# Optimization experiments

Hardware: AMD Instinct MI355X
Metric: run time of the kernel (lower is better)

The kernel has to match this reference:

```python
import jax, jax.numpy as jnp
import numpy as np

IN_CH = [32, 48, 96, 136, 232]
SIZES = [128, 64, 32, 16, 8]
C = 256      # FPN channels (compound_coef=0)
A = 9        # anchors per location
NC = 10      # num_classes
B = 8
BN_EPS = 1e-5


def conv2d(x, w, b, pad):
    # x: [B,Cin,H,W], w: [Cout,Cin,kh,kw]
    y = jax.lax.conv_general_dilated(
        x, w, window_strides=(1, 1), padding=[(pad, pad), (pad, pad)],
        dimension_numbers=("NCHW", "OIHW", "NCHW"))
    return y + b[None, :, None, None]


def bn_eval(x, g, bt, m, v):
    inv = g / jnp.sqrt(v + BN_EPS)
    return x * inv[None, :, None, None] + (bt - m * inv)[None, :, None, None]


def upsample_nearest(x, th, tw):
    fh = th // x.shape[2]
    fw = tw // x.shape[3]
    return jnp.repeat(jnp.repeat(x, fh, axis=2), fw, axis=3)


def run_head(feats, w1, b1, g, bt, m, v, w2, b2, out_dim):
    outs = []
    for f in feats:
        h = jax.nn.relu(bn_eval(conv2d(f, w1, b1, 1), g, bt, m, v))
        h = conv2d(h, w2, b2, 0)                       # [B, A*out_dim, H, W]
        Bb, _, H, W = h.shape
        h = h.transpose(0, 2, 3, 1).reshape(Bb, H * W * A, out_dim)
        outs.append(h)
    return jnp.concatenate(outs, axis=1)               # [B, total_anchors, out_dim]


def _forward(f1, f2, f3, f4, f5,
             lat_w1, lat_w2, lat_w3, lat_w4, lat_w5, lat_b,
             fpn_w, fpn_b,
             cls_w1, cls_b1, cls_g, cls_bt, cls_m, cls_v, cls_w2, cls_b2,
             reg_w1, reg_b1, reg_g, reg_bt, reg_m, reg_v, reg_w2, reg_b2):
    feats = [f1, f2, f3, f4, f5]
    lat_ws = [lat_w1, lat_w2, lat_w3, lat_w4, lat_w5]
    # lateral 1x1 convs
    laterals = [conv2d(feats[i], lat_ws[i], lat_b[i], 0) for i in range(5)]
    # top-down pathway with nearest upsampling
    for i in range(4, 0, -1):
        th, tw = laterals[i - 1].shape[2], laterals[i - 1].shape[3]
        laterals[i - 1] = laterals[i - 1] + upsample_nearest(laterals[i], th, tw)
    # 3x3 fpn convs
    fpn_feats = [conv2d(laterals[i], fpn_w[i], fpn_b[i], 1) for i in range(5)]
    cls = run_head(fpn_feats, cls_w1, cls_b1, cls_g, cls_bt, cls_m, cls_v, cls_w2, cls_b2, NC)
    reg = run_head(fpn_feats, reg_w1, reg_b1, reg_g, reg_bt, reg_m, reg_v, reg_w2, reg_b2, 4)
    return jnp.concatenate([reg, cls], axis=2)          # [B, total_anchors, 4+NC]


def setup_inputs() -> dict:
    key = jax.random.key(0)
    ks = jax.random.split(key, 16)
    d = {}
    for i, (ch, s) in enumerate(zip(IN_CH, SIZES)):
        d[f"f{i+1}"] = jax.random.normal(ks[i], (B, ch, s, s), jnp.float32)
    for i, ch in enumerate(IN_CH):
        std = float(np.sqrt(2.0 / C))
        d[f"lat_w{i+1}"] = jax.random.normal(ks[5 + i], (C, ch, 1, 1), jnp.float32) * std
    d["lat_b"] = jnp.zeros((5, C), jnp.float32)
    d["fpn_w"] = jax.random.normal(ks[10], (5, C, C, 3, 3), jnp.float32) * float(np.sqrt(2.0 / (9 * C)))
    d["fpn_b"] = jnp.zeros((5, C), jnp.float32)
    d["cls_w1"] = jax.random.normal(ks[11], (C, C, 3, 3), jnp.float32) * float(np.sqrt(2.0 / (9 * C)))
    d["cls_b1"] = jnp.zeros((C,), jnp.float32)
    d["cls_g"] = jnp.ones((C,), jnp.float32)
    d["cls_bt"] = jnp.zeros((C,), jnp.float32)
    d["cls_m"] = jnp.zeros((C,), jnp.float32)
    d["cls_v"] = jnp.ones((C,), jnp.float32)
    d["cls_w2"] = jax.random.normal(ks[12], (A * NC, C, 1, 1), jnp.float32) * float(np.sqrt(2.0 / (A * NC)))
    d["cls_b2"] = jnp.zeros((A * NC,), jnp.float32)
    d["reg_w1"] = jax.random.normal(ks[13], (C, C, 3, 3), jnp.float32) * float(np.sqrt(2.0 / (9 * C)))
    d["reg_b1"] = jnp.zeros((C,), jnp.float32)
    d["reg_g"] = jnp.ones((C,), jnp.float32)
    d["reg_bt"] = jnp.zeros((C,), jnp.float32)
    d["reg_m"] = jnp.zeros((C,), jnp.float32)
    d["reg_v"] = jnp.ones((C,), jnp.float32)
    d["reg_w2"] = jax.random.normal(ks[14], (A * 4, C, 1, 1), jnp.float32) * float(np.sqrt(2.0 / (A * 4)))
    d["reg_b2"] = jnp.zeros((A * 4,), jnp.float32)
    return d


def reference(f1, f2, f3, f4, f5,
              lat_w1, lat_w2, lat_w3, lat_w4, lat_w5, lat_b,
              fpn_w, fpn_b,
              cls_w1, cls_b1, cls_g, cls_bt, cls_m, cls_v, cls_w2, cls_b2,
              reg_w1, reg_b1, reg_g, reg_bt, reg_m, reg_v, reg_w2, reg_b2):
    return _forward(f1, f2, f3, f4, f5,
                    lat_w1, lat_w2, lat_w3, lat_w4, lat_w5, lat_b,
                    fpn_w, fpn_b,
                    cls_w1, cls_b1, cls_g, cls_bt, cls_m, cls_v, cls_w2, cls_b2,
                    reg_w1, reg_b1, reg_g, reg_bt, reg_m, reg_v, reg_w2, reg_b2)
```

## Files before the change

kernel.cpp:

```cpp
#include <hip/hip_runtime.h>


typedef unsigned short ush;
typedef __attribute__((ext_vector_type(8))) short v8s;
typedef __attribute__((ext_vector_type(4))) float v4f;

constexpr int TOTAL_ANCH = 196416;

#define VMW(n) asm volatile("s_waitcnt vmcnt(" #n ")" ::: "memory")
#define LGW()  asm volatile("s_waitcnt lgkmcnt(0)" ::: "memory")

__device__ __forceinline__ ush f2bf(float x) {
    unsigned u = __builtin_bit_cast(unsigned, x);
    u += 0x7FFFu + ((u >> 16) & 1u);
    return (ush)(u >> 16);
}
__device__ __forceinline__ float bf2f(ush h) {
    unsigned u = ((unsigned)h) << 16;
    return __builtin_bit_cast(float, u);
}
__device__ __forceinline__ void splitf(float x, ush& hi, ush& lo) {
    hi = f2bf(x);
    lo = f2bf(x - bf2f(hi));
}

__device__ __forceinline__ void gl_lds16(const ush* g, short* l) {
    __builtin_amdgcn_global_load_lds(
        (const __attribute__((address_space(1))) unsigned*)(const void*)g,
        (__attribute__((address_space(3))) unsigned*)l, 16, 0, 0);
}

struct Lvl3 {
    const ush* xh; const ush* xl;
    ush* yh; ush* yl;
    const float* bias;
    int wofs, logS, logHW, bstart;
};
struct Tab3 { Lvl3 l[4]; };

struct LvlS {
    const ush* xh; const ush* xl;
    int abase, logHW, bstart, ibase;
};
struct TabS { LvlS l[4]; };

template <int OM, bool BNR>
__global__ __launch_bounds__(512, 2)
void conv3f(Tab3 T,
            const ush* __restrict__ Wh, const ush* __restrict__ Wl,
            const float* __restrict__ bng, const float* __restrict__ bnb,
            const float* __restrict__ bnm, const float* __restrict__ bnv)
{
    constexpr int K = 2304, KC = 72;

    const int nwg = gridDim.x;
    const int flat = blockIdx.x;
    const int xcd = flat & 7, sidx = flat >> 3;
    const int q = nwg >> 3, r8 = nwg & 7;
    const int nf = (xcd < r8 ? xcd * (q + 1) : r8 * (q + 1) + (xcd - r8) * q) + sidx;

    int li = 0;
    if (nf >= T.l[1].bstart) li = 1;
    if (nf >= T.l[2].bstart) li = 2;
    if (nf >= T.l[3].bstart) li = 3;
    const int logS = T.l[li].logS, logHW = T.l[li].logHW;
    const int S = 1 << logS, HW = 1 << logHW, P = S + 2;
    const ush* __restrict__ Xh = T.l[li].xh;
    const ush* __restrict__ Xl = T.l[li].xl;
    ush* __restrict__ Yh = T.l[li].yh;
    ush* __restrict__ Yl = T.l[li].yl;
    const float* __restrict__ bias = T.l[li].bias;
    const int wofs = T.l[li].wofs;
    const int n0 = (nf - T.l[li].bstart) * 128;

    __shared__ __align__(16) short lds[3][24576];

    const int tid = threadIdx.x;
    const int lane = tid & 63, w = tid >> 6;
    const int wm = w & 3, wn = w >> 2;
    const int l15 = lane & 15, l4 = lane >> 4;
    const int lr = lane >> 2, ls = lane & 3;
    const int sw = ls ^ ((lr >> 1) & 3);

    const int role = w >> 1, part = w & 1;
    const ush* gsrc = role == 0 ? Wh + wofs : role == 1 ? Wl + wofs
                    : role == 2 ? Xh : Xl;
    const int poff = role < 2 ? role * 8192 : 16384 + (role - 2) * 4096;

    int sb[8];
    if (role < 2) {
#pragma unroll
        for (int t = 0; t < 8; ++t)
            sb[t] = (part * 128 + t * 16 + lr) * K + sw * 8;
    } else {
#pragma unroll
        for (int t = 0; t < 4; ++t) {
            const int p = n0 + part * 64 + t * 16 + lr;
            const int bb = p >> logHW, hw = p & (HW - 1);
            const int oh = hw >> logS, ow = hw & (S - 1);
            sb[t] = ((bb * P + oh + 1) * P + ow + 1) * 256 + sw * 8;
        }
    }

    auto stage = [&](int u, int c, int h) {
        short* db = &lds[0][0] + u * 24576 + poff;
        if (role < 2) {
            const int coff = c * 32;
#pragma unroll
            for (int k = 0; k < 4; ++k) {
                const int t = h * 4 + k;
                gl_lds16(gsrc + (sb[t] + coff), db + part * 4096 + t * 512);
            }
        } else {
            const int rs = c >> 3;
            const int rr = (rs * 11) >> 5;
            const int ss = rs - 3 * rr;
            const int coff = ((rr - 1) * P + (ss - 1)) * 256 + (c & 7) * 32;
#pragma unroll
            for (int k = 0; k < 2; ++k) {
                const int t = h * 2 + k;
                gl_lds16(gsrc + (sb[t] + coff), db + part * 2048 + t * 512);
            }
        }
    };

    const int slr = (l4 ^ ((l15 >> 1) & 3)) * 8;
    int aoff[4], boff[4];
#pragma unroll
    for (int i = 0; i < 4; ++i) aoff[i] = (wm * 64 + i * 16 + l15) * 32 + slr;
#pragma unroll
    for (int j = 0; j < 4; ++j) boff[j] = (wn * 64 + j * 16 + l15) * 32 + slr;

    v4f acc[4][4] = {};

    stage(0, 0, 0); stage(0, 0, 1);
    stage(1, 1, 0); stage(1, 1, 1);
    if (role < 2) { VMW(8); } else { VMW(4); }
    __builtin_amdgcn_sched_barrier(0);
    __builtin_amdgcn_s_barrier();

    int cur = 0, nst = 2;
    for (int c = 0; c < KC; ++c) {
        const bool pf = (c + 2) < KC;
        const short* bb = &lds[0][0] + cur * 24576;

        v8s ah[4], al[4], bh[4], bl[4];
#pragma unroll
        for (int i = 0; i < 4; ++i) {
            ah[i] = *(const v8s*)(bb + aoff[i]);
            al[i] = *(const v8s*)(bb + 8192 + aoff[i]);
        }
#pragma unroll
        for (int j = 0; j < 2; ++j) {
            bh[j] = *(const v8s*)(bb + 16384 + boff[j]);
            bl[j] = *(const v8s*)(bb + 20480 + boff[j]);
        }
        if (pf) stage(nst, c + 2, 0);
        __builtin_amdgcn_s_barrier();
        LGW();
        __builtin_amdgcn_sched_barrier(0);
        __builtin_amdgcn_s_setprio(1);
#pragma unroll
        for (int j = 0; j < 2; ++j)
#pragma unroll
            for (int i = 0; i < 4; ++i) {
                acc[i][j] = __builtin_amdgcn_mfma_f32_16x16x32_bf16(ah[i], bh[j], acc[i][j], 0, 0, 0);
                acc[i][j] = __builtin_amdgcn_mfma_f32_16x16x32_bf16(ah[i], bl[j], acc[i][j], 0, 0, 0);
                acc[i][j] = __builtin_amdgcn_mfma_f32_16x16x32_bf16(al[i], bh[j], acc[i][j], 0, 0, 0);
            }
        __builtin_amdgcn_s_setprio(0);
        __builtin_amdgcn_s_barrier();

#pragma unroll
        for (int j = 2; j < 4; ++j) {
            bh[j] = *(const v8s*)(bb + 16384 + boff[j]);
            bl[j] = *(const v8s*)(bb + 20480 + boff[j]);
        }
        if (pf) stage(nst, c + 2, 1);
        __builtin_amdgcn_s_barrier();
        LGW();
        __builtin_amdgcn_sched_barrier(0);
        __builtin_amdgcn_s_setprio(1);
#pragma unroll
        for (int j = 2; j < 4; ++j)
#pragma unroll
            for (int i = 0; i < 4; ++i) {
                acc[i][j] = __builtin_amdgcn_mfma_f32_16x16x32_bf16(ah[i], bh[j], acc[i][j], 0, 0, 0);
                acc[i][j] = __builtin_amdgcn_mfma_f32_16x16x32_bf16(ah[i], bl[j], acc[i][j], 0, 0, 0);
                acc[i][j] = __builtin_amdgcn_mfma_f32_16x16x32_bf16(al[i], bh[j], acc[i][j], 0, 0, 0);
            }
        __builtin_amdgcn_s_setprio(0);
        if (pf) { if (role < 2) { VMW(8); } else { VMW(4); } }
        else    { VMW(0); }
        __builtin_amdgcn_sched_barrier(0);
        __builtin_amdgcn_s_barrier();

        cur = cur == 2 ? 0 : cur + 1;
        nst = nst == 2 ? 0 : nst + 1;
    }

#pragma unroll
    for (int i = 0; i < 4; ++i) {
        const int co = wm * 64 + i * 16 + l4 * 4;
        float sc[4], sh[4];
#pragma unroll
        for (int e = 0; e < 4; ++e) {
            if (BNR) {
                const float inv = bng[co + e] * rsqrtf(bnv[co + e] + 1e-5f);
                sc[e] = inv;
                sh[e] = (bias[co + e] - bnm[co + e]) * inv + bnb[co + e];
            } else { sc[e] = 1.f; sh[e] = bias[co + e]; }
        }
#pragma unroll
        for (int j = 0; j < 4; ++j) {
            const int ncol = n0 + wn * 64 + j * 16 + l15;
            const int b  = ncol >> logHW;
            const int hw = ncol & (HW - 1);
            float val[4];
#pragma unroll
            for (int e = 0; e < 4; ++e) {
                float x = acc[i][j][e] * sc[e] + sh[e];
                if (BNR) x = fmaxf(x, 0.f);
                val[e] = x;
            }
            int pidx;
            if (OM == 0) {
                const int oh = hw >> logS, ow = hw & (S - 1);
                pidx = (b * P + oh + 1) * P + ow + 1;
            } else {
                pidx = ncol;
            }
            const int addr = pidx * 256 + co;
            ush hs[4], ls2[4];
#pragma unroll
            for (int e = 0; e < 4; ++e) splitf(val[e], hs[e], ls2[e]);
            *(uint2*)&Yh[addr] = make_uint2(hs[0] | ((unsigned)hs[1] << 16),
                                            hs[2] | ((unsigned)hs[3] << 16));
            *(uint2*)&Yl[addr] = make_uint2(ls2[0] | ((unsigned)ls2[1] << 16),
                                            ls2[2] | ((unsigned)ls2[3] << 16));
        }
    }
}

template <int DD>
__global__ __launch_bounds__(256, 3)
void conv_sf(TabS T, const ush* __restrict__ Wh, const ush* __restrict__ Wl,
             const float* __restrict__ bias, float* __restrict__ out)
{
    constexpr int K = 256, KC = 8, Cout = 9 * DD;
    constexpr int coloff = (DD == 10) ? 4 : 0;

    const int nwg = gridDim.x;
    const int flat = blockIdx.x;
    const int xcd = flat & 7, sidx = flat >> 3;
    const int q = nwg >> 3, r8 = nwg & 7;
    const int nf = (xcd < r8 ? xcd * (q + 1) : r8 * (q + 1) + (xcd - r8) * q) + sidx;

    int li = 0;
    if (nf >= T.l[1].bstart) li = 1;
    if (nf >= T.l[2].bstart) li = 2;
    if (nf >= T.l[3].bstart) li = 3;
    const int logHW = T.l[li].logHW;
    const int HW = 1 << logHW;
    const ush* __restrict__ Xh = T.l[li].xh;
    const ush* __restrict__ Xl = T.l[li].xl;
    const int abase = T.l[li].abase, ibase = T.l[li].ibase;
    const int n0 = (nf - T.l[li].bstart) * 128;

    __shared__ short lds[4][128][32];

    const int tid = threadIdx.x;
    const int lane = tid & 63;
    const int w = tid >> 6;
    const int wm = w & 1, wn = w >> 1;
    const int l15 = lane & 15, l4 = lane >> 4;
    const int lr = lane >> 2, ls = lane & 3;
    const int sw = ls ^ ((lr >> 1) & 3);
    const ush* gsrc = (w == 0) ? Wh : (w == 1) ? Wl : (w == 2) ? Xh : Xl;
    int sb[8];
    if (w < 2) {
#pragma unroll
        for (int t = 0; t < 8; ++t)
            sb[t] = (t * 16 + lr) * K + sw * 8;
    } else {
#pragma unroll
        for (int t = 0; t < 8; ++t)
            sb[t] = (n0 + t * 16 + lr) * 256 + sw * 8;
    }
    short* mypl = &lds[w][0][0];
    const int slA = (l4 ^ ((l15 >> 1) & 3)) * 8;

    v4f acc[4][4] = {};

    for (int c = 0; c < KC; ++c) {
        const int coff = c * 32;
#pragma unroll
        for (int t = 0; t < 8; ++t)
            gl_lds16(gsrc + (sb[t] + coff), mypl + t * 512);

        __syncthreads();

        v8s ah[4], al[4];
#pragma unroll
        for (int i = 0; i < 4; ++i) {
            ah[i] = *(const v8s*)&lds[0][wm * 64 + i * 16 + l15][slA];
            al[i] = *(const v8s*)&lds[1][wm * 64 + i * 16 + l15][slA];
        }
#pragma unroll
        for (int j = 0; j < 4; ++j) {
            const v8s bh = *(const v8s*)&lds[2][wn * 64 + j * 16 + l15][slA];
            const v8s bl = *(const v8s*)&lds[3][wn * 64 + j * 16 + l15][slA];
#pragma unroll
            for (int i = 0; i < 4; ++i) {
                acc[i][j] = __builtin_amdgcn_mfma_f32_16x16x32_bf16(ah[i], bh, acc[i][j], 0, 0, 0);
                acc[i][j] = __builtin_amdgcn_mfma_f32_16x16x32_bf16(ah[i], bl, acc[i][j], 0, 0, 0);
                acc[i][j] = __builtin_amdgcn_mfma_f32_16x16x32_bf16(al[i], bh, acc[i][j], 0, 0, 0);
            }
        }
        __syncthreads();
    }

#pragma unroll
    for (int i = 0; i < 4; ++i) {
        const int co = wm * 64 + i * 16 + l4 * 4;
        float sh[4];
#pragma unroll
        for (int e = 0; e < 4; ++e)
            sh[e] = (co + e < Cout) ? bias[co + e] : 0.f;
#pragma unroll
        for (int j = 0; j < 4; ++j) {
            const int ncol = n0 + wn * 64 + j * 16 + l15;
            const int b  = ncol >> logHW;
            const int hw = ncol & (HW - 1);
#pragma unroll
            for (int e = 0; e < 4; ++e) {
                const int c2 = co + e;
                if (c2 < Cout) {
                    const float val = acc[i][j][e] + sh[e];
                    const int a = c2 / DD, cl = c2 - a * DD;
                    out[(size_t)((b + ibase) * TOTAL_ANCH + abase + hw * 9 + a) * 14
                        + coloff + cl] = val;
                }
            }
        }
    }
}

template <int KS, int OM, bool BNR, int DD>
__global__ __launch_bounds__(256, 3)
void conv_mfma(const ush* __restrict__ Xh, const ush* __restrict__ Xl,
               const ush* __restrict__ Wh, const ush* __restrict__ Wl,
               const float* __restrict__ bias,
               ush* __restrict__ Yh, ush* __restrict__ Yl,
               int K, int logS, int logHW, int Kin)
{
    const int tid = threadIdx.x;

    const int nwg  = gridDim.x * gridDim.y;
    const int flat = blockIdx.y * gridDim.x + blockIdx.x;
    const int xcd = flat & 7, sidx = flat >> 3;
    const int q = nwg >> 3, r8 = nwg & 7;
    const int nf = (xcd < r8 ? xcd * (q + 1) : r8 * (q + 1) + (xcd - r8) * q) + sidx;
    int bx, by;
    if (gridDim.y == 2) { bx = nf >> 1; by = nf & 1; }
    else                { bx = nf;      by = 0;      }

    const int n0  = bx * 128;
    const int co0 = by * 128;
    const int S = 1 << logS, HW = 1 << logHW, P = S + 2;

    __shared__ short lds[4][128][32];

    const int lane = tid & 63;
    const int w = tid >> 6;
    const int wm = w & 1, wn = w >> 1;
    const int l15 = lane & 15, l4 = lane >> 4;

    const int lr = lane >> 2, ls = lane & 3;
    const int sw = ls ^ ((lr >> 1) & 3);
    const ush* gsrc = (w == 0) ? Wh : (w == 1) ? Wl : (w == 2) ? Xh : Xl;
    int sb[8];
    if (w < 2) {
#pragma unroll
        for (int t = 0; t < 8; ++t)
            sb[t] = (co0 + t * 16 + lr) * K + sw * 8;
    } else {
#pragma unroll
        for (int t = 0; t < 8; ++t) {
            const int p = n0 + t * 16 + lr;
            sb[t] = p * Kin + sw * 8;
        }
    }
    short* mypl = &lds[w][0][0];

    const int KC = K >> 5;
    const int slA = (l4 ^ ((l15 >> 1) & 3)) * 8;

    v4f acc[4][4] = {};

    for (int c = 0; c < KC; ++c) {
        const int coff = c * 32;
#pragma unroll
        for (int t = 0; t < 8; ++t)
            gl_lds16(gsrc + (sb[t] + coff), mypl + t * 512);

        __syncthreads();

        v8s ah[4], al[4];
#pragma unroll
        for (int i = 0; i < 4; ++i) {
            ah[i] = *(const v8s*)&lds[0][wm * 64 + i * 16 + l15][slA];
            al[i] = *(const v8s*)&lds[1][wm * 64 + i * 16 + l15][slA];
        }
#pragma unroll
        for (int j = 0; j < 4; ++j) {
            const v8s bh = *(const v8s*)&lds[2][wn * 64 + j * 16 + l15][slA];
            const v8s bl = *(const v8s*)&lds[3][wn * 64 + j * 16 + l15][slA];
#pragma unroll
            for (int i = 0; i < 4; ++i) {
                acc[i][j] = __builtin_amdgcn_mfma_f32_16x16x32_bf16(ah[i], bh, acc[i][j], 0, 0, 0);
                acc[i][j] = __builtin_amdgcn_mfma_f32_16x16x32_bf16(ah[i], bl, acc[i][j], 0, 0, 0);
                acc[i][j] = __builtin_amdgcn_mfma_f32_16x16x32_bf16(al[i], bh, acc[i][j], 0, 0, 0);
            }
        }
        __syncthreads();
    }

#pragma unroll
    for (int i = 0; i < 4; ++i) {
        const int cob = wm * 64 + i * 16 + l4 * 4;
        const int co  = co0 + cob;
        float sh[4];
#pragma unroll
        for (int e = 0; e < 4; ++e) sh[e] = bias[co + e];
#pragma unroll
        for (int j = 0; j < 4; ++j) {
            const int ncol = n0 + wn * 64 + j * 16 + l15;
            const int b  = ncol >> logHW;
            const int hw = ncol & (HW - 1);
            float val[4];
#pragma unroll
            for (int e = 0; e < 4; ++e) val[e] = acc[i][j][e] + sh[e];
            int pidx;
            if (OM == 0) {
                const int oh = hw >> logS, ow = hw & (S - 1);
                pidx = (b * P + oh + 1) * P + ow + 1;
            } else {
                pidx = ncol;
            }
            const int addr = pidx * 256 + co;
            ush hs[4], ls2[4];
#pragma unroll
            for (int e = 0; e < 4; ++e) splitf(val[e], hs[e], ls2[e]);
            *(uint2*)&Yh[addr] = make_uint2(hs[0] | ((unsigned)hs[1] << 16),
                                            hs[2] | ((unsigned)hs[3] << 16));
            *(uint2*)&Yl[addr] = make_uint2(ls2[0] | ((unsigned)ls2[1] << 16),
                                            ls2[2] | ((unsigned)ls2[3] << 16));
        }
    }
}


__global__ void w3_prep(const float* __restrict__ W, ush* __restrict__ wh,
                        ush* __restrict__ wl, int total) {
    const int idx = blockIdx.x * 256 + threadIdx.x;
    if (idx >= total) return;
    const int co5 = idx / 2304;
    const int kk  = idx - co5 * 2304;
    const int rs = kk >> 8, ci = kk & 255;
    splitf(W[(co5 * 256 + ci) * 9 + rs], wh[idx], wl[idx]);
}

__global__ void w1_prep(const float* __restrict__ W, ush* __restrict__ wh,
                        ush* __restrict__ wl, int Cin, int Kp, int Cout, int total) {
    const int idx = blockIdx.x * 256 + threadIdx.x;
    if (idx >= total) return;
    const int co = idx / Kp;
    const int k  = idx - co * Kp;
    const float x = (co < Cout && k < Cin) ? W[co * Cin + k] : 0.f;
    splitf(x, wh[idx], wl[idx]);
}

__global__ void in_prep(const float* __restrict__ f, ush* __restrict__ xh,
                        ush* __restrict__ xl, int Cin, int Kp, int logHW, int total) {
    const int idx = blockIdx.x * 256 + threadIdx.x;
    if (idx >= total) return;
    const int c = idx % Kp;
    const int n = idx / Kp;
    const int b  = n >> logHW;
    const int hw = n & ((1 << logHW) - 1);
    const float x = (c < Cin) ? f[((b * Cin + c) << logHW) + hw] : 0.f;
    splitf(x, xh[idx], xl[idx]);
}

__global__ void upsample_hl(ush* __restrict__ fh, ush* __restrict__ fl,
                            const ush* __restrict__ ch, const ush* __restrict__ cl2,
                            int logSf, int total) {
    const int idx = blockIdx.x * 256 + threadIdx.x;
    if (idx >= total) return;
    const int ci = idx & 255;
    const int r  = idx >> 8;
    const int Sf = 1 << logSf;
    const int wf = r & (Sf - 1);
    const int hf = (r >> logSf) & (Sf - 1);
    const int b  = r >> (2 * logSf);
    const int Pf = Sf + 2, Pc = (Sf >> 1) + 2;
    const int fi = ((b * Pf + hf + 1) * Pf + wf + 1) * 256 + ci;
    const int cx = ((b * Pc + (hf >> 1) + 1) * Pc + (wf >> 1) + 1) * 256 + ci;
    const float x = bf2f(fh[fi]) + bf2f(fl[fi]) + bf2f(ch[cx]) + bf2f(cl2[cx]);
    splitf(x, fh[fi], fl[fi]);
}

__global__ void ring_zero(ush* __restrict__ yh, ush* __restrict__ yl, int S, int total) {
    const int idx = blockIdx.x * 256 + threadIdx.x;
    if (idx >= total) return;
    const int ci = idx & 255;
    const int r  = idx >> 8;
    const int P = S + 2;
    const int ring = 4 * P - 4;
    const int pr = r % ring;
    const int b  = r / ring;
    int ph, pw;
    if (pr < P)            { ph = 0;     pw = pr; }
    else if (pr < 2 * P)   { ph = P - 1; pw = pr - P; }
    else { const int q = pr - 2 * P; ph = 1 + (q >> 1); pw = (q & 1) ? (P - 1) : 0; }
    const int a = ((b * P + ph) * P + pw) * 256 + ci;
    yh[a] = 0; yl[a] = 0;
}


extern "C" void kernel_launch(void* const* d_in, const int* in_sizes, int n_in,
                              void* d_out, int out_size, void* d_ws, size_t ws_size,
                              hipStream_t stream)
{
    const float* f[5];     const float* lat_w[5];
    for (int i = 0; i < 5; ++i) f[i] = (const float*)d_in[i];
    for (int i = 0; i < 5; ++i) lat_w[i] = (const float*)d_in[5 + i];
    const float* lat_b  = (const float*)d_in[10];
    const float* fpn_w  = (const float*)d_in[11];
    const float* fpn_b  = (const float*)d_in[12];
    const float* cls_w1 = (const float*)d_in[13];
    const float* cls_b1 = (const float*)d_in[14];
    const float* cls_g  = (const float*)d_in[15];
    const float* cls_bt = (const float*)d_in[16];
    const float* cls_m  = (const float*)d_in[17];
    const float* cls_v  = (const float*)d_in[18];
    const float* cls_w2 = (const float*)d_in[19];
    const float* cls_b2 = (const float*)d_in[20];
    const float* reg_w1 = (const float*)d_in[21];
    const float* reg_b1 = (const float*)d_in[22];
    const float* reg_g  = (const float*)d_in[23];
    const float* reg_bt = (const float*)d_in[24];
    const float* reg_m  = (const float*)d_in[25];
    const float* reg_v  = (const float*)d_in[26];
    const float* reg_w2 = (const float*)d_in[27];
    const float* reg_b2 = (const float*)d_in[28];

    float* out = (float*)d_out;
    ush*   ws16 = (ush*)d_ws;

    static const int S_[5]     = {128, 64, 32, 16, 8};
    static const int logS_[5]  = {7, 6, 5, 4, 3};
    static const int logHW_[5] = {14, 12, 10, 8, 6};
    static const int HW_[5]    = {16384, 4096, 1024, 256, 64};
    static const int Cin_[5]   = {32, 48, 96, 136, 232};
    static const int Kp_[5]    = {32, 64, 96, 160, 256};
    static const int abase_[5] = {0, 147456, 184320, 193536, 195840};
    constexpr int BIG = 0x7fffffff;

    size_t off = 0;
    auto alloc = [&](size_t elems) {
        ush* p = ws16 + off;
        off += (elems + 63) & ~(size_t)63;
        return p;
    };

    ush *lat_h[5], *lat_l[5];
    for (int i = 0; i < 5; ++i) {
        const int P = S_[i] + 2;
        const size_t e = (size_t)2048 * P * P;
        lat_h[i] = alloc(e); lat_l[i] = alloc(e);
    }
    const size_t lat_bytes = off * sizeof(ush);

    const size_t ARENA_E = (size_t)2 * 4 * 130 * 130 * 256;
    ush* arena = alloc(ARENA_E);

    ush* fw_h = alloc((size_t)5 * 256 * 2304); ush* fw_l = alloc((size_t)5 * 256 * 2304);
    ush* cw_h = alloc(256 * 2304);             ush* cw_l = alloc(256 * 2304);
    ush* rw_h = alloc(256 * 2304);             ush* rw_l = alloc(256 * 2304);
    ush *lw_h[5], *lw_l[5];
    for (int i = 0; i < 5; ++i) { lw_h[i] = alloc(256 * Kp_[i]); lw_l[i] = alloc(256 * Kp_[i]); }
    ush* c2_h = alloc(128 * 256); ush* c2_l = alloc(128 * 256);
    ush* r2_h = alloc(128 * 256); ush* r2_l = alloc(128 * 256);

    hipMemsetAsync(ws16, 0, lat_bytes, stream);

    {
        int t = 5 * 256 * 2304;
        w3_prep<<<dim3((t + 255) / 256), 256, 0, stream>>>(fpn_w, fw_h, fw_l, t);
        t = 256 * 2304;
        w3_prep<<<dim3((t + 255) / 256), 256, 0, stream>>>(cls_w1, cw_h, cw_l, t);
        w3_prep<<<dim3((t + 255) / 256), 256, 0, stream>>>(reg_w1, rw_h, rw_l, t);
        for (int i = 0; i < 5; ++i) {
            t = 256 * Kp_[i];
            w1_prep<<<dim3((t + 255) / 256), 256, 0, stream>>>(lat_w[i], lw_h[i], lw_l[i], Cin_[i], Kp_[i], 256, t);
        }
        t = 128 * 256;
        w1_prep<<<dim3((t + 255) / 256), 256, 0, stream>>>(cls_w2, c2_h, c2_l, 256, 256, 90, t);
        w1_prep<<<dim3((t + 255) / 256), 256, 0, stream>>>(reg_w2, r2_h, r2_l, 256, 256, 36, t);
    }

    for (int i = 0; i < 5; ++i) {
        const int N = 8 * HW_[i];
        const int t = N * Kp_[i];
        ush* xh = arena;
        ush* xl = arena + (size_t)N * Kp_[i];
        in_prep<<<dim3((t + 255) / 256), 256, 0, stream>>>(f[i], xh, xl, Cin_[i], Kp_[i], logHW_[i], t);
        conv_mfma<1, 0, false, 0><<<dim3(N / 128, 2), 256, 0, stream>>>(
            xh, xl, lw_h[i], lw_l[i], lat_b + i * 256,
            lat_h[i], lat_l[i],
            Kp_[i], logS_[i], logHW_[i], Kp_[i]);
    }

    for (int i = 4; i >= 1; --i) {
        const int t = 8 * HW_[i - 1] * 256;
        upsample_hl<<<dim3((t + 255) / 256), 256, 0, stream>>>(
            lat_h[i - 1], lat_l[i - 1], lat_h[i], lat_l[i], logS_[i - 1], t);
    }

    ush *fpn_h4[5], *fpn_l4[5];
    {
        size_t o = 0;
        for (int i = 1; i < 5; ++i) {
            const int P = S_[i] + 2;
            fpn_h4[i] = arena + o; o += (size_t)2048 * P * P;
            fpn_l4[i] = arena + o; o += (size_t)2048 * P * P;
        }
    }
    for (int i = 1; i < 5; ++i) {
        const int P = S_[i] + 2;
        const int rt = 8 * (4 * P - 4) * 256;
        ring_zero<<<dim3((rt + 255) / 256), 256, 0, stream>>>(fpn_h4[i], fpn_l4[i], S_[i], rt);
    }
    static const int bstart4[4] = {0, 256, 320, 336};

    {
        Tab3 T{};
        for (int k = 0; k < 4; ++k) {
            const int i = k + 1;
            T.l[k] = Lvl3{ lat_h[i], lat_l[i], fpn_h4[i], fpn_l4[i],
                           fpn_b + i * 256, i * 256 * 2304,
                           logS_[i], logHW_[i], bstart4[k] };
        }
        conv3f<0, false><<<dim3(340), 512, 0, stream>>>(
            T, fw_h, fw_l, nullptr, nullptr, nullptr, nullptr);
    }
    {
        Tab3 T{};
        for (int k = 0; k < 4; ++k) {
            const int i = k + 1;
            T.l[k] = Lvl3{ fpn_h4[i], fpn_l4[i], lat_h[i], lat_l[i],
                           cls_b1, 0, logS_[i], logHW_[i], bstart4[k] };
        }
        conv3f<1, true><<<dim3(340), 512, 0, stream>>>(
            T, cw_h, cw_l, cls_g, cls_bt, cls_m, cls_v);
    }
    {
        TabS T{};
        for (int k = 0; k < 4; ++k) {
            const int i = k + 1;
            T.l[k] = LvlS{ lat_h[i], lat_l[i], abase_[i], logHW_[i], bstart4[k], 0 };
        }
        conv_sf<10><<<dim3(340), 256, 0, stream>>>(T, c2_h, c2_l, cls_b2, out);
    }
    {
        Tab3 T{};
        for (int k = 0; k < 4; ++k) {
            const int i = k + 1;
            T.l[k] = Lvl3{ fpn_h4[i], fpn_l4[i], lat_h[i], lat_l[i],
                           reg_b1, 0, logS_[i], logHW_[i], bstart4[k] };
        }
        conv3f<1, true><<<dim3(340), 512, 0, stream>>>(
            T, rw_h, rw_l, reg_g, reg_bt, reg_m, reg_v);
    }
    {
        TabS T{};
        for (int k = 0; k < 4; ++k) {
            const int i = k + 1;
            T.l[k] = LvlS{ lat_h[i], lat_l[i], abase_[i], logHW_[i], bstart4[k], 0 };
        }
        conv_sf<4><<<dim3(340), 256, 0, stream>>>(T, r2_h, r2_l, reg_b2, out);
    }

    {
        const int P = 130;
        const size_t padg = (size_t)4 * P * P * 256;
        const size_t unpg = (size_t)4 * 16384 * 256;
        for (int g = 0; g < 2; ++g) {
            ush* fpn_h = arena;
            ush* fpn_l = arena + padg;
            ush* lat0p_h = lat_h[0] + (size_t)g * padg;
            ush* lat0p_l = lat_l[0] + (size_t)g * padg;
            ush* tmp_h   = lat_h[0] + (size_t)g * unpg;
            ush* tmp_l   = lat_l[0] + (size_t)g * unpg;
            const int rt = 4 * (4 * P - 4) * 256;
            ring_zero<<<dim3((rt + 255) / 256), 256, 0, stream>>>(fpn_h, fpn_l, 128, rt);

            Tab3 T{};
            T.l[0] = Lvl3{ lat0p_h, lat0p_l, fpn_h, fpn_l, fpn_b, 0, 7, 14, 0 };
            for (int k = 1; k < 4; ++k) T.l[k].bstart = BIG;
            conv3f<0, false><<<dim3(512), 512, 0, stream>>>(
                T, fw_h, fw_l, nullptr, nullptr, nullptr, nullptr);

            Tab3 Tc{};
            Tc.l[0] = Lvl3{ fpn_h, fpn_l, tmp_h, tmp_l, cls_b1, 0, 7, 14, 0 };
            for (int k = 1; k < 4; ++k) Tc.l[k].bstart = BIG;
            conv3f<1, true><<<dim3(512), 512, 0, stream>>>(
                Tc, cw_h, cw_l, cls_g, cls_bt, cls_m, cls_v);

            TabS Ts{};
            Ts.l[0] = LvlS{ tmp_h, tmp_l, 0, 14, 0, 4 * g };
            for (int k = 1; k < 4; ++k) Ts.l[k].bstart = BIG;
            conv_sf<10><<<dim3(512), 256, 0, stream>>>(Ts, c2_h, c2_l, cls_b2, out);

            Tab3 Tr{};
            Tr.l[0] = Lvl3{ fpn_h, fpn_l, tmp_h, tmp_l, reg_b1, 0, 7, 14, 0 };
            for (int k = 1; k < 4; ++k) Tr.l[k].bstart = BIG;
            conv3f<1, true><<<dim3(512), 512, 0, stream>>>(
                Tr, rw_h, rw_l, reg_g, reg_bt, reg_m, reg_v);

            TabS Tq{};
            Tq.l[0] = LvlS{ tmp_h, tmp_l, 0, 14, 0, 4 * g };
            for (int k = 1; k < 4; ++k) Tq.l[k].bstart = BIG;
            conv_sf<4><<<dim3(512), 256, 0, stream>>>(Tq, r2_h, r2_l, reg_b2, out);
        }
    }
}
```

Measured before the change: 2.727 ms.

## Enlarge conv3 tile to 256x256 with double-buffered LDS and quadrant MFMA phases

```diff
diff --git a/kernel.cpp b/kernel.cpp
--- a/kernel.cpp
+++ b/kernel.cpp
@@ -44,14 +44,47 @@
 };
 struct TabS { LvlS l[4]; };
 
+#define MFMA3(AH, AL, BH, BL, ACC)                                            \
+    ACC = __builtin_amdgcn_mfma_f32_16x16x32_bf16(AH, BH, ACC, 0, 0, 0);      \
+    ACC = __builtin_amdgcn_mfma_f32_16x16x32_bf16(AH, BL, ACC, 0, 0, 0);      \
+    ACC = __builtin_amdgcn_mfma_f32_16x16x32_bf16(AL, BH, ACC, 0, 0, 0);
+
+#define RDA(BP, IB)                                                           \
+    _Pragma("unroll")                                                         \
+    for (int i = 0; i < 4; ++i) {                                             \
+        a_h[i] = *(const v8s*)((BP) + abA + ((IB) + i) * 512);                \
+        a_l[i] = *(const v8s*)((BP) + abA + 8192 + ((IB) + i) * 512);         \
+    }
+
+#define RDB(BP, JB)                                                           \
+    _Pragma("unroll")                                                         \
+    for (int j = 0; j < 2; ++j) {                                             \
+        b_h[j] = *(const v8s*)((BP) + abB + ((JB) + j) * 512);                \
+        b_l[j] = *(const v8s*)((BP) + abB + 8192 + ((JB) + j) * 512);         \
+    }
+
+#define PHASE(IB, JB)                                                         \
+    LGW();                                                                    \
+    __builtin_amdgcn_sched_barrier(0);                                        \
+    __builtin_amdgcn_s_setprio(1);                                            \
+    _Pragma("unroll")                                                         \
+    for (int j = 0; j < 2; ++j) {                                             \
+        _Pragma("unroll")                                                     \
+        for (int i = 0; i < 4; ++i) {                                         \
+            MFMA3(a_h[i], a_l[i], b_h[j], b_l[j], acc[(IB) + i][(JB) + j]);   \
+        }                                                                     \
+    }                                                                         \
+    __builtin_amdgcn_s_setprio(0);
+
 template <int OM, bool BNR>
 __global__ __launch_bounds__(512, 2)
-void conv3f(Tab3 T,
+void conv3g(Tab3 T,
             const ush* __restrict__ Wh, const ush* __restrict__ Wl,
             const float* __restrict__ bng, const float* __restrict__ bnb,
             const float* __restrict__ bnm, const float* __restrict__ bnv)
 {
     constexpr int K = 2304, KC = 72;
+    constexpr int BUFS = 32768;
 
     const int nwg = gridDim.x;
     const int flat = blockIdx.x;
@@ -71,13 +104,13 @@
     ush* __restrict__ Yl = T.l[li].yl;
     const float* __restrict__ bias = T.l[li].bias;
     const int wofs = T.l[li].wofs;
-    const int n0 = (nf - T.l[li].bstart) * 128;
-
-    __shared__ __align__(16) short lds[3][24576];
+    const int n0 = (nf - T.l[li].bstart) * 256;
+
+    __shared__ __align__(16) short lds[2][BUFS];
 
     const int tid = threadIdx.x;
     const int lane = tid & 63, w = tid >> 6;
-    const int wm = w & 3, wn = w >> 2;
+    const int wm = w & 1, wn = w >> 1;
     const int l15 = lane & 15, l4 = lane >> 4;
     const int lr = lane >> 2, ls = lane & 3;
     const int sw = ls ^ ((lr >> 1) & 3);
@@ -85,7 +118,7 @@
     const int role = w >> 1, part = w & 1;
     const ush* gsrc = role == 0 ? Wh + wofs : role == 1 ? Wl + wofs
                     : role == 2 ? Xh : Xl;
-    const int poff = role < 2 ? role * 8192 : 16384 + (role - 2) * 4096;
+    const int poff = role * 8192 + part * 4096;
 
     int sb[8];
     if (role < 2) {
@@ -94,114 +127,64 @@
             sb[t] = (part * 128 + t * 16 + lr) * K + sw * 8;
     } else {
 #pragma unroll
-        for (int t = 0; t < 4; ++t) {
-            const int p = n0 + part * 64 + t * 16 + lr;
+        for (int t = 0; t < 8; ++t) {
+            const int p = n0 + part * 128 + t * 16 + lr;
             const int bb = p >> logHW, hw = p & (HW - 1);
             const int oh = hw >> logS, ow = hw & (S - 1);
             sb[t] = ((bb * P + oh + 1) * P + ow + 1) * 256 + sw * 8;
         }
     }
 
-    auto stage = [&](int u, int c, int h) {
-        short* db = &lds[0][0] + u * 24576 + poff;
-        if (role < 2) {
-            const int coff = c * 32;
-#pragma unroll
-            for (int k = 0; k < 4; ++k) {
-                const int t = h * 4 + k;
-                gl_lds16(gsrc + (sb[t] + coff), db + part * 4096 + t * 512);
-            }
-        } else {
+    auto stage = [&](int u, int c) {
+        short* db = &lds[0][0] + u * BUFS + poff;
+        int coff;
+        if (role < 2) coff = c * 32;
+        else {
             const int rs = c >> 3;
             const int rr = (rs * 11) >> 5;
             const int ss = rs - 3 * rr;
-            const int coff = ((rr - 1) * P + (ss - 1)) * 256 + (c & 7) * 32;
-#pragma unroll
-            for (int k = 0; k < 2; ++k) {
-                const int t = h * 2 + k;
-                gl_lds16(gsrc + (sb[t] + coff), db + part * 2048 + t * 512);
-            }
-        }
+            coff = ((rr - 1) * P + (ss - 1)) * 256 + (c & 7) * 32;
+        }
+#pragma unroll
+        for (int t = 0; t < 8; ++t)
+            gl_lds16(gsrc + (sb[t] + coff), db + t * 512);
     };
 
     const int slr = (l4 ^ ((l15 >> 1) & 3)) * 8;
-    int aoff[4], boff[4];
-#pragma unroll
-    for (int i = 0; i < 4; ++i) aoff[i] = (wm * 64 + i * 16 + l15) * 32 + slr;
-#pragma unroll
-    for (int j = 0; j < 4; ++j) boff[j] = (wn * 64 + j * 16 + l15) * 32 + slr;
-
-    v4f acc[4][4] = {};
-
-    stage(0, 0, 0); stage(0, 0, 1);
-    stage(1, 1, 0); stage(1, 1, 1);
-    if (role < 2) { VMW(8); } else { VMW(4); }
+    const int abA = (wm * 128 + l15) * 32 + slr;
+    const int abB = 16384 + (wn * 64 + l15) * 32 + slr;
+
+    v4f acc[8][4] = {};
+    v8s a_h[4], a_l[4], b_h[2], b_l[2];
+
+    stage(0, 0);
+    VMW(0);
     __builtin_amdgcn_sched_barrier(0);
     __builtin_amdgcn_s_barrier();
 
-    int cur = 0, nst = 2;
+    int cur = 0;
     for (int c = 0; c < KC; ++c) {
-        const bool pf = (c + 2) < KC;
-        const short* bb = &lds[0][0] + cur * 24576;
-
-        v8s ah[4], al[4], bh[4], bl[4];
-#pragma unroll
-        for (int i = 0; i < 4; ++i) {
-            ah[i] = *(const v8s*)(bb + aoff[i]);
-            al[i] = *(const v8s*)(bb + 8192 + aoff[i]);
-        }
-#pragma unroll
-        for (int j = 0; j < 2; ++j) {
-            bh[j] = *(const v8s*)(bb + 16384 + boff[j]);
-            bl[j] = *(const v8s*)(bb + 20480 + boff[j]);
-        }
-        if (pf) stage(nst, c + 2, 0);
-        __builtin_amdgcn_s_barrier();
-        LGW();
-        __builtin_amdgcn_sched_barrier(0);
-        __builtin_amdgcn_s_setprio(1);
-#pragma unroll
-        for (int j = 0; j < 2; ++j)
-#pragma unroll
-            for (int i = 0; i < 4; ++i) {
-                acc[i][j] = __builtin_amdgcn_mfma_f32_16x16x32_bf16(ah[i], bh[j], acc[i][j], 0, 0, 0);
-                acc[i][j] = __builtin_amdgcn_mfma_f32_16x16x32_bf16(ah[i], bl[j], acc[i][j], 0, 0, 0);
-                acc[i][j] = __builtin_amdgcn_mfma_f32_16x16x32_bf16(al[i], bh[j], acc[i][j], 0, 0, 0);
-            }
-        __builtin_amdgcn_s_setprio(0);
-        __builtin_amdgcn_s_barrier();
-
-#pragma unroll
-        for (int j = 2; j < 4; ++j) {
-            bh[j] = *(const v8s*)(bb + 16384 + boff[j]);
-            bl[j] = *(const v8s*)(bb + 20480 + boff[j]);
-        }
-        if (pf) stage(nst, c + 2, 1);
-        __builtin_amdgcn_s_barrier();
-        LGW();
-        __builtin_amdgcn_sched_barrier(0);
-        __builtin_amdgcn_s_setprio(1);
-#pragma unroll
-        for (int j = 2; j < 4; ++j)
-#pragma unroll
-            for (int i = 0; i < 4; ++i) {
-                acc[i][j] = __builtin_amdgcn_mfma_f32_16x16x32_bf16(ah[i], bh[j], acc[i][j], 0, 0, 0);
-                acc[i][j] = __builtin_amdgcn_mfma_f32_16x16x32_bf16(ah[i], bl[j], acc[i][j], 0, 0, 0);
-                acc[i][j] = __builtin_amdgcn_mfma_f32_16x16x32_bf16(al[i], bh[j], acc[i][j], 0, 0, 0);
-            }
-        __builtin_amdgcn_s_setprio(0);
-        if (pf) { if (role < 2) { VMW(8); } else { VMW(4); } }
-        else    { VMW(0); }
+        if (c + 1 < KC) stage(cur ^ 1, c + 1);
+        const short* bp = &lds[0][0] + cur * BUFS;
+
+        RDA(bp, 0); RDB(bp, 0);
+        PHASE(0, 0);
+        RDA(bp, 4);
+        PHASE(4, 0);
+        RDB(bp, 2);
+        PHASE(4, 2);
+        RDA(bp, 0);
+        PHASE(0, 2);
+
+        if (c + 1 < KC) VMW(0);
         __builtin_amdgcn_sched_barrier(0);
         __builtin_amdgcn_s_barrier();
-
-        cur = cur == 2 ? 0 : cur + 1;
-        nst = nst == 2 ? 0 : nst + 1;
-    }
-
-#pragma unroll
-    for (int i = 0; i < 4; ++i) {
-        const int co = wm * 64 + i * 16 + l4 * 4;
+        cur ^= 1;
+    }
+
+#pragma unroll
+    for (int i = 0; i < 8; ++i) {
+        const int co = wm * 128 + i * 16 + l4 * 4;
         float sc[4], sh[4];
 #pragma unroll
         for (int e = 0; e < 4; ++e) {
@@ -643,7 +626,8 @@
         const int rt = 8 * (4 * P - 4) * 256;
         ring_zero<<<dim3((rt + 255) / 256), 256, 0, stream>>>(fpn_h4[i], fpn_l4[i], S_[i], rt);
     }
-    static const int bstart4[4] = {0, 256, 320, 336};
+    static const int bstart4[4] = {0, 128, 160, 168};
+    static const int bstartS[4] = {0, 256, 320, 336};
 
     {
         Tab3 T{};
@@ -653,7 +637,7 @@
                            fpn_b + i * 256, i * 256 * 2304,
                            logS_[i], logHW_[i], bstart4[k] };
         }
-        conv3f<0, false><<<dim3(340), 512, 0, stream>>>(
+        conv3g<0, false><<<dim3(170), 512, 0, stream>>>(
             T, fw_h, fw_l, nullptr, nullptr, nullptr, nullptr);
     }
     {
@@ -663,14 +647,14 @@
             T.l[k] = Lvl3{ fpn_h4[i], fpn_l4[i], lat_h[i], lat_l[i],
                            cls_b1, 0, logS_[i], logHW_[i], bstart4[k] };
         }
-        conv3f<1, true><<<dim3(340), 512, 0, stream>>>(
+        conv3g<1, true><<<dim3(170), 512, 0, stream>>>(
             T, cw_h, cw_l, cls_g, cls_bt, cls_m, cls_v);
     }
     {
         TabS T{};
         for (int k = 0; k < 4; ++k) {
             const int i = k + 1;
-            T.l[k] = LvlS{ lat_h[i], lat_l[i], abase_[i], logHW_[i], bstart4[k], 0 };
+            T.l[k] = LvlS{ lat_h[i], lat_l[i], abase_[i], logHW_[i], bstartS[k], 0 };
         }
         conv_sf<10><<<dim3(340), 256, 0, stream>>>(T, c2_h, c2_l, cls_b2, out);
     }
@@ -681,14 +665,14 @@
             T.l[k] = Lvl3{ fpn_h4[i], fpn_l4[i], lat_h[i], lat_l[i],
                            reg_b1, 0, logS_[i], logHW_[i], bstart4[k] };
         }
-        conv3f<1, true><<<dim3(340), 512, 0, stream>>>(
+        conv3g<1, true><<<dim3(170), 512, 0, stream>>>(
             T, rw_h, rw_l, reg_g, reg_bt, reg_m, reg_v);
     }
     {
         TabS T{};
         for (int k = 0; k < 4; ++k) {
             const int i = k + 1;
-            T.l[k] = LvlS{ lat_h[i], lat_l[i], abase_[i], logHW_[i], bstart4[k], 0 };
+            T.l[k] = LvlS{ lat_h[i], lat_l[i], abase_[i], logHW_[i], bstartS[k], 0 };
         }
         conv_sf<4><<<dim3(340), 256, 0, stream>>>(T, r2_h, r2_l, reg_b2, out);
     }
@@ -710,13 +694,13 @@
             Tab3 T{};
             T.l[0] = Lvl3{ lat0p_h, lat0p_l, fpn_h, fpn_l, fpn_b, 0, 7, 14, 0 };
             for (int k = 1; k < 4; ++k) T.l[k].bstart = BIG;
-            conv3f<0, false><<<dim3(512), 512, 0, stream>>>(
+            conv3g<0, false><<<dim3(256), 512, 0, stream>>>(
                 T, fw_h, fw_l, nullptr, nullptr, nullptr, nullptr);
 
             Tab3 Tc{};
             Tc.l[0] = Lvl3{ fpn_h, fpn_l, tmp_h, tmp_l, cls_b1, 0, 7, 14, 0 };
             for (int k = 1; k < 4; ++k) Tc.l[k].bstart = BIG;
-            conv3f<1, true><<<dim3(512), 512, 0, stream>>>(
+            conv3g<1, true><<<dim3(256), 512, 0, stream>>>(
                 Tc, cw_h, cw_l, cls_g, cls_bt, cls_m, cls_v);
 
             TabS Ts{};
@@ -727,7 +711,7 @@
             Tab3 Tr{};
             Tr.l[0] = Lvl3{ fpn_h, fpn_l, tmp_h, tmp_l, reg_b1, 0, 7, 14, 0 };
             for (int k = 1; k < 4; ++k) Tr.l[k].bstart = BIG;
-            conv3f<1, true><<<dim3(512), 512, 0, stream>>>(
+            conv3g<1, true><<<dim3(256), 512, 0, stream>>>(
                 Tr, rw_h, rw_l, reg_g, reg_bt, reg_m, reg_v);
 
             TabS Tq{};
```

Measured after the change: 2.396 ms. 12.1% less time.
